# Kernel tuning notes

Measured on AMD Instinct MI355X. Metric: run time of the kernel, lower is better.

The kernel has to match this reference:

```python
import jax, jax.numpy as jnp
import numpy as np

# Constants from init_kwargs
NODE_BUDGET = 200.0
ALPHA = 0.5
COS_EPS = 1e-6

N, F = 200000, 256   # num_nodes, num_features
B = 1024             # batch_size (roots)
M = 500000           # candidate (u, batch) pairs this hop
E = 2000000          # frontier->candidate edges


def setup_inputs() -> dict:
    key = jax.random.key(0)
    ks = jax.random.split(key, 12)
    bound = 1.0 / np.sqrt(F)
    return {
        "x": jax.random.normal(ks[0], (N, F), dtype=jnp.float32),
        "w_ego_root": jax.random.uniform(ks[1], (F,), minval=-bound, maxval=bound, dtype=jnp.float32),
        "w_ego_u": jax.random.uniform(ks[2], (F,), minval=-bound, maxval=bound, dtype=jnp.float32),
        "w_layer_v": jax.random.uniform(ks[3], (F,), minval=-bound, maxval=bound, dtype=jnp.float32),
        "w_layer_u": jax.random.uniform(ks[4], (F,), minval=-bound, maxval=bound, dtype=jnp.float32),
        "n_imp": jax.random.uniform(ks[5], (N,), dtype=jnp.float32),
        "budgets": jnp.ones((B,), dtype=jnp.float32) * NODE_BUDGET,
        "batch_nodes": jax.random.randint(ks[6], (B,), 0, N, dtype=jnp.int32),
        "u_ids": jax.random.randint(ks[7], (M,), 0, N, dtype=jnp.int32),
        "batch_ptr": jnp.sort(jax.random.randint(ks[8], (M,), 0, B, dtype=jnp.int32)),
        "edge_src": jax.random.randint(ks[9], (E,), 0, B, dtype=jnp.int32),
        "edge_dst": jax.random.randint(ks[10], (E,), 0, M, dtype=jnp.int32),
    }


def reference(x, w_ego_root, w_ego_u, w_layer_v, w_layer_u, n_imp, budgets,
              batch_nodes, u_ids, batch_ptr, edge_src, edge_dst):
    # One hop of AdaptiveSampler.batch_wise_sampling score computation.
    # h_roots = x[batch_nodes] * w_ego_root  -> [B, F]
    x_roots = x[batch_nodes]                       # [B, F] gather
    h_roots = x_roots * w_ego_root                 # [B, F]
    xu = x[u_ids]                                  # [M, F] gather (dominant traffic)
    hu = xu * w_ego_u                              # [M, F]
    hr = h_roots[batch_ptr]                        # [M, F] gather

    # ego_score = cosine(h_roots[batch_ptr], x[u] * w_ego_u)
    dot = jnp.sum(hr * hu, axis=-1)                # [M]
    nr = jnp.linalg.norm(hr, axis=-1)
    nu = jnp.linalg.norm(hu, axis=-1)
    ego_score = dot / (jnp.maximum(nr, COS_EPS) * jnp.maximum(nu, COS_EPS))

    # layer_kernel: frontier projection scattered onto candidates via adjacency,
    # combined with the candidate projection (assumed tanh combine; see notes).
    sv = x_roots @ w_layer_v                       # [B]
    agg = jax.ops.segment_sum(sv[edge_src], edge_dst, num_segments=M)  # [M]
    su = xu @ w_layer_u                            # [M]
    layer_score = jnp.tanh(agg + su)               # [M]

    # p_u = (a*ego + (1-a)*layer) * n_imp[u] * (budget/node_budget)
    p_u = (ALPHA * ego_score + (1.0 - ALPHA) * layer_score) \
          * n_imp[u_ids] * (budgets[batch_ptr] / NODE_BUDGET)

    # per-batch normalizer (detached in original: .clone().detach())
    p_norm = jax.lax.stop_gradient(
        jax.ops.segment_max(p_u, batch_ptr, num_segments=B))  # [B]
    p_u = p_u / p_norm[batch_ptr] + 1.0
    # replace_nan(p_u, nan_to=0.0, inf_to=1.0)
    p_u = jnp.where(jnp.isnan(p_u), 0.0, jnp.where(jnp.isinf(p_u), 1.0, p_u))
    # p_clip = clamp(p_u, 1e-5, 1)
    p_clip = jnp.clip(p_u, 1e-5, 1.0)
    return p_clip
```

## Files before the change

kernel.cpp:

```cpp
#include <hip/hip_runtime.h>

#define F 256
#define NODE_BUDGET 200.0f
#define COS_EPS 1e-6f

__global__ __launch_bounds__(256) void root_kernel(
    const float* __restrict__ x,
    const float* __restrict__ w_ego_root,
    const float* __restrict__ w_ego_u,
    const float* __restrict__ w_layer_v,
    const float* __restrict__ budgets,
    const int* __restrict__ batch_nodes,
    float* __restrict__ g, float* __restrict__ nr,
    float* __restrict__ sv, float* __restrict__ bscale)
{
    __shared__ float red[2][4];
    int b = blockIdx.x;
    int f = threadIdx.x;
    int root = batch_nodes[b];
    float xf = x[(size_t)root * F + f];
    float hr = xf * w_ego_root[f];
    g[(size_t)b * F + f] = hr * w_ego_u[f];
    float a = hr * hr;
    float c = xf * w_layer_v[f];
    #pragma unroll
    for (int off = 32; off; off >>= 1) {
        a += __shfl_xor(a, off);
        c += __shfl_xor(c, off);
    }
    int lane = f & 63, wv = f >> 6;
    if (lane == 0) { red[0][wv] = a; red[1][wv] = c; }
    __syncthreads();
    if (f == 0) {
        float as = red[0][0] + red[0][1] + red[0][2] + red[0][3];
        float cs = red[1][0] + red[1][1] + red[1][2] + red[1][3];
        nr[b] = sqrtf(as);
        sv[b] = cs;
        bscale[b] = budgets[b] * (1.0f / NODE_BUDGET);
    }
}

__global__ __launch_bounds__(256) void edge_kernel(
    const int* __restrict__ edge_src, const int* __restrict__ edge_dst,
    const float* __restrict__ sv, float* __restrict__ agg, int E)
{
    int i = blockIdx.x * 256 + threadIdx.x;
    int stride = gridDim.x * 256;
    for (; i < E; i += stride)
        atomicAdd(&agg[edge_dst[i]], sv[edge_src[i]]);
}

__global__ __launch_bounds__(256) void cand_kernel(
    const float* __restrict__ x,
    const int* __restrict__ u_ids, const int* __restrict__ batch_ptr,
    const float* __restrict__ g, const float* __restrict__ nr,
    const float* __restrict__ bscale, const float* __restrict__ agg,
    const float* __restrict__ w_ego_u, const float* __restrict__ w_layer_u,
    const float* __restrict__ n_imp,
    float* __restrict__ p_out, int M)
{
    int tid = threadIdx.x;
    int lane = tid & 63;
    int sub = lane >> 4;
    int sl = lane & 15;
    int m = blockIdx.x * 16 + (tid >> 6) * 4 + sub;
    if (m >= M) return;
    int u = u_ids[m];
    int b = batch_ptr[m];
    const float4* xr = (const float4*)(x + (size_t)u * F);
    const float4* gr = (const float4*)(g + (size_t)b * F);
    const float4* weu = (const float4*)w_ego_u;
    const float4* wlu = (const float4*)w_layer_u;
    float acc = 0.0f;
    float a2  = 0.0f;
    float su  = 0.0f;
    #pragma unroll
    for (int p = 0; p < 4; ++p) {
        float4 xv = xr[p * 16 + sl];
        float4 gv = gr[p * 16 + sl];
        float4 wu = weu[p * 16 + sl];
        float4 wl = wlu[p * 16 + sl];
        acc += xv.x * gv.x + xv.y * gv.y + xv.z * gv.z + xv.w * gv.w;
        float h0 = xv.x * wu.x, h1 = xv.y * wu.y, h2 = xv.z * wu.z, h3 = xv.w * wu.w;
        a2  += h0 * h0 + h1 * h1 + h2 * h2 + h3 * h3;
        su  += xv.x * wl.x + xv.y * wl.y + xv.z * wl.z + xv.w * wl.w;
    }
    #pragma unroll
    for (int off = 8; off; off >>= 1) {
        acc += __shfl_xor(acc, off);
        a2  += __shfl_xor(a2, off);
        su  += __shfl_xor(su, off);
    }
    if (sl == 0) {
        float nu = sqrtf(a2);
        float ego = acc / (fmaxf(nr[b], COS_EPS) * fmaxf(nu, COS_EPS));
        float layer = tanhf(agg[m] + su);
        float p = (0.5f * ego + 0.5f * layer) * n_imp[u] * bscale[b];
        p_out[m] = p;
    }
}

__global__ __launch_bounds__(256) void seg_norm_kernel(
    const int* __restrict__ batch_ptr, float* __restrict__ out, int M)
{
    int b = blockIdx.x;
    int lo = 0, hi = M;
    while (lo < hi) { int mid = (lo + hi) >> 1; if (batch_ptr[mid] < b) lo = mid + 1; else hi = mid; }
    int start = lo;
    hi = M;
    while (lo < hi) { int mid = (lo + hi) >> 1; if (batch_ptr[mid] <= b) lo = mid + 1; else hi = mid; }
    int end = lo;
    float mx = -INFINITY;
    for (int i = start + threadIdx.x; i < end; i += 256)
        mx = fmaxf(mx, out[i]);
    #pragma unroll
    for (int off = 32; off; off >>= 1)
        mx = fmaxf(mx, __shfl_xor(mx, off));
    __shared__ float red[4];
    __shared__ float s_pn;
    int lane = threadIdx.x & 63, wv = threadIdx.x >> 6;
    if (lane == 0) red[wv] = mx;
    __syncthreads();
    if (threadIdx.x == 0)
        s_pn = fmaxf(fmaxf(red[0], red[1]), fmaxf(red[2], red[3]));
    __syncthreads();
    float pn = s_pn;
    for (int i = start + threadIdx.x; i < end; i += 256) {
        float v = out[i] / pn + 1.0f;
        if (isnan(v)) v = 0.0f;
        else if (isinf(v)) v = 1.0f;
        out[i] = fminf(fmaxf(v, 1e-5f), 1.0f);
    }
}

extern "C" void kernel_launch(void* const* d_in, const int* in_sizes, int n_in,
                              void* d_out, int out_size, void* d_ws, size_t ws_size,
                              hipStream_t stream) {
    const float* x          = (const float*)d_in[0];
    const float* w_ego_root = (const float*)d_in[1];
    const float* w_ego_u    = (const float*)d_in[2];
    const float* w_layer_v  = (const float*)d_in[3];
    const float* w_layer_u  = (const float*)d_in[4];
    const float* n_imp      = (const float*)d_in[5];
    const float* budgets    = (const float*)d_in[6];
    const int* batch_nodes = (const int*)d_in[7];
    const int* u_ids       = (const int*)d_in[8];
    const int* batch_ptr   = (const int*)d_in[9];
    const int* edge_src    = (const int*)d_in[10];
    const int* edge_dst    = (const int*)d_in[11];
    float* out = (float*)d_out;

    int B = in_sizes[7];
    int M = in_sizes[8];
    int E = in_sizes[10];

    float* ws = (float*)d_ws;
    size_t off = 0;
    float* agg = ws + off;                          off += (size_t)((M + 3) & ~3);
    size_t zero_bytes = off * sizeof(float);
    float* g       = ws + off;                      off += (size_t)B * F;
    float* nr      = ws + off;                      off += (size_t)((B + 3) & ~3);
    float* sv      = ws + off;                      off += (size_t)((B + 3) & ~3);
    float* bscale  = ws + off;                      off += (size_t)((B + 3) & ~3);

    hipMemsetAsync(d_ws, 0, zero_bytes, stream);

    root_kernel<<<B, 256, 0, stream>>>(x, w_ego_root, w_ego_u, w_layer_v,
                                       budgets, batch_nodes, g, nr, sv, bscale);
    edge_kernel<<<2048, 256, 0, stream>>>(edge_src, edge_dst, sv, agg, E);
    cand_kernel<<<(M + 15) / 16, 256, 0, stream>>>(x, u_ids, batch_ptr, g, nr,
                                                   bscale, agg, w_ego_u, w_layer_u,
                                                   n_imp, out, M);
    seg_norm_kernel<<<B, 256, 0, stream>>>(batch_ptr, out, M);
}
```

Measured before the change: 465.4 us.

## Group candidates by node via linked lists to reuse each x row

Builds per-node linked lists of candidate indices with atomicExch, then runs one 16-lane group per node. Each group loads the node's feature row once, computes its norm and layer projection once, and walks the list to compute the cosine against each root row. This cuts repeated gathers of x rows: with M=500k draws over N=200k nodes, many rows are duplicated, and the old path re-read x once per candidate. In exchange it adds a list-building pass, an extra memset, and serial pointer-chasing with uneven per-node work. Precomputing the inverse root norm is a small extra change.

```diff
diff --git a/kernel.cpp b/kernel.cpp
--- a/kernel.cpp
+++ b/kernel.cpp
@@ -11,7 +11,7 @@
     const float* __restrict__ w_layer_v,
     const float* __restrict__ budgets,
     const int* __restrict__ batch_nodes,
-    float* __restrict__ g, float* __restrict__ nr,
+    float* __restrict__ g, float* __restrict__ nrinv,
     float* __restrict__ sv, float* __restrict__ bscale)
 {
     __shared__ float red[2][4];
@@ -34,10 +34,20 @@
     if (f == 0) {
         float as = red[0][0] + red[0][1] + red[0][2] + red[0][3];
         float cs = red[1][0] + red[1][1] + red[1][2] + red[1][3];
-        nr[b] = sqrtf(as);
+        nrinv[b] = 1.0f / fmaxf(sqrtf(as), COS_EPS);
         sv[b] = cs;
         bscale[b] = budgets[b] * (1.0f / NODE_BUDGET);
     }
+}
+
+__global__ __launch_bounds__(256) void build_lists_kernel(
+    const int* __restrict__ u_ids, int* __restrict__ head,
+    int* __restrict__ next, int M)
+{
+    int i = blockIdx.x * 256 + threadIdx.x;
+    if (i >= M) return;
+    int u = u_ids[i];
+    next[i] = atomicExch(&head[u], i);
 }
 
 __global__ __launch_bounds__(256) void edge_kernel(
@@ -50,53 +60,68 @@
         atomicAdd(&agg[edge_dst[i]], sv[edge_src[i]]);
 }
 
-__global__ __launch_bounds__(256) void cand_kernel(
+__global__ __launch_bounds__(256) void cand_list_kernel(
     const float* __restrict__ x,
-    const int* __restrict__ u_ids, const int* __restrict__ batch_ptr,
-    const float* __restrict__ g, const float* __restrict__ nr,
+    const int* __restrict__ head, const int* __restrict__ next,
+    const int* __restrict__ batch_ptr,
+    const float* __restrict__ g, const float* __restrict__ nrinv,
     const float* __restrict__ bscale, const float* __restrict__ agg,
     const float* __restrict__ w_ego_u, const float* __restrict__ w_layer_u,
     const float* __restrict__ n_imp,
-    float* __restrict__ p_out, int M)
+    float* __restrict__ p_out, int N)
 {
     int tid = threadIdx.x;
     int lane = tid & 63;
     int sub = lane >> 4;
     int sl = lane & 15;
-    int m = blockIdx.x * 16 + (tid >> 6) * 4 + sub;
-    if (m >= M) return;
-    int u = u_ids[m];
-    int b = batch_ptr[m];
-    const float4* xr = (const float4*)(x + (size_t)u * F);
-    const float4* gr = (const float4*)(g + (size_t)b * F);
+    int n = blockIdx.x * 16 + (tid >> 6) * 4 + sub;
+    if (n >= N) return;
+    int m = head[n];
+    if (m < 0) return;
+
+    const float4* xr  = (const float4*)(x + (size_t)n * F);
     const float4* weu = (const float4*)w_ego_u;
     const float4* wlu = (const float4*)w_layer_u;
-    float acc = 0.0f;
-    float a2  = 0.0f;
-    float su  = 0.0f;
-    #pragma unroll
-    for (int p = 0; p < 4; ++p) {
-        float4 xv = xr[p * 16 + sl];
-        float4 gv = gr[p * 16 + sl];
-        float4 wu = weu[p * 16 + sl];
-        float4 wl = wlu[p * 16 + sl];
-        acc += xv.x * gv.x + xv.y * gv.y + xv.z * gv.z + xv.w * gv.w;
-        float h0 = xv.x * wu.x, h1 = xv.y * wu.y, h2 = xv.z * wu.z, h3 = xv.w * wu.w;
-        a2  += h0 * h0 + h1 * h1 + h2 * h2 + h3 * h3;
-        su  += xv.x * wl.x + xv.y * wl.y + xv.z * wl.z + xv.w * wl.w;
+
+    float4 xv0 = xr[sl], xv1 = xr[16 + sl], xv2 = xr[32 + sl], xv3 = xr[48 + sl];
+    float a2 = 0.0f, su = 0.0f;
+    {
+        float4 wu, wl, xv;
+        #define ACCUM(XV, P) \
+            xv = XV; wu = weu[(P)*16 + sl]; wl = wlu[(P)*16 + sl]; \
+            { float h0 = xv.x*wu.x, h1 = xv.y*wu.y, h2 = xv.z*wu.z, h3 = xv.w*wu.w; \
+              a2 += h0*h0 + h1*h1 + h2*h2 + h3*h3; \
+              su += xv.x*wl.x + xv.y*wl.y + xv.z*wl.z + xv.w*wl.w; }
+        ACCUM(xv0, 0) ACCUM(xv1, 1) ACCUM(xv2, 2) ACCUM(xv3, 3)
+        #undef ACCUM
     }
     #pragma unroll
     for (int off = 8; off; off >>= 1) {
-        acc += __shfl_xor(acc, off);
-        a2  += __shfl_xor(a2, off);
-        su  += __shfl_xor(su, off);
-    }
-    if (sl == 0) {
-        float nu = sqrtf(a2);
-        float ego = acc / (fmaxf(nr[b], COS_EPS) * fmaxf(nu, COS_EPS));
-        float layer = tanhf(agg[m] + su);
-        float p = (0.5f * ego + 0.5f * layer) * n_imp[u] * bscale[b];
-        p_out[m] = p;
+        a2 += __shfl_xor(a2, off);
+        su += __shfl_xor(su, off);
+    }
+    float inv_nu = 1.0f / fmaxf(sqrtf(a2), COS_EPS);
+    float imp = n_imp[n];
+
+    while (m >= 0) {
+        int mn = next[m];
+        int b = batch_ptr[m];
+        float ag = agg[m];
+        const float4* gr = (const float4*)(g + (size_t)b * F);
+        float4 g0 = gr[sl], g1 = gr[16 + sl], g2 = gr[32 + sl], g3 = gr[48 + sl];
+        float acc = xv0.x*g0.x + xv0.y*g0.y + xv0.z*g0.z + xv0.w*g0.w
+                  + xv1.x*g1.x + xv1.y*g1.y + xv1.z*g1.z + xv1.w*g1.w
+                  + xv2.x*g2.x + xv2.y*g2.y + xv2.z*g2.z + xv2.w*g2.w
+                  + xv3.x*g3.x + xv3.y*g3.y + xv3.z*g3.z + xv3.w*g3.w;
+        #pragma unroll
+        for (int off = 8; off; off >>= 1)
+            acc += __shfl_xor(acc, off);
+        if (sl == 0) {
+            float ego = acc * inv_nu * nrinv[b];
+            float layer = tanhf(ag + su);
+            p_out[m] = (0.5f * ego + 0.5f * layer) * imp * bscale[b];
+        }
+        m = mn;
     }
 }
 
@@ -150,6 +175,7 @@
     const int* edge_dst    = (const int*)d_in[11];
     float* out = (float*)d_out;
 
+    int N = in_sizes[5];
     int B = in_sizes[7];
     int M = in_sizes[8];
     int E = in_sizes[10];
@@ -159,17 +185,22 @@
     float* agg = ws + off;                          off += (size_t)((M + 3) & ~3);
     size_t zero_bytes = off * sizeof(float);
     float* g       = ws + off;                      off += (size_t)B * F;
-    float* nr      = ws + off;                      off += (size_t)((B + 3) & ~3);
+    float* nrinv   = ws + off;                      off += (size_t)((B + 3) & ~3);
     float* sv      = ws + off;                      off += (size_t)((B + 3) & ~3);
     float* bscale  = ws + off;                      off += (size_t)((B + 3) & ~3);
+    int* head      = (int*)(ws + off);              off += (size_t)((N + 3) & ~3);
+    int* next      = (int*)(ws + off);              off += (size_t)((M + 3) & ~3);
 
     hipMemsetAsync(d_ws, 0, zero_bytes, stream);
+    hipMemsetAsync(head, 0xFF, (size_t)N * sizeof(int), stream);
 
     root_kernel<<<B, 256, 0, stream>>>(x, w_ego_root, w_ego_u, w_layer_v,
-                                       budgets, batch_nodes, g, nr, sv, bscale);
+                                       budgets, batch_nodes, g, nrinv, sv, bscale);
+    build_lists_kernel<<<(M + 255) / 256, 256, 0, stream>>>(u_ids, head, next, M);
     edge_kernel<<<2048, 256, 0, stream>>>(edge_src, edge_dst, sv, agg, E);
-    cand_kernel<<<(M + 15) / 16, 256, 0, stream>>>(x, u_ids, batch_ptr, g, nr,
-                                                   bscale, agg, w_ego_u, w_layer_u,
-                                                   n_imp, out, M);
+    cand_list_kernel<<<(N + 15) / 16, 256, 0, stream>>>(x, head, next, batch_ptr,
+                                                        g, nrinv, bscale, agg,
+                                                        w_ego_u, w_layer_u, n_imp,
+                                                        out, N);
     seg_norm_kernel<<<B, 256, 0, stream>>>(batch_ptr, out, M);
 }
```

New measurement: 487.6 us. 4.8% more time.

## Bucket candidates by node id to improve cache locality of x row gathers

Applied to the files above, without the earlier changes.

Adds a scatter pass that buckets candidate indices into 32-node groups, using fixed-capacity slots plus an overflow list. The candidate kernel then walks this permutation, so rows of x for nearby node ids are read close together in time and can hit in L2/MALL instead of costing random HBM traffic. It also precomputes the reciprocal root norm. The price is an extra atomic scatter kernel, a memset of the perm buffer, many idle lanes from empty slots (S = 6250*128 = 800k slots for 500k items), and scattered writes to p_out.

```diff
diff --git a/kernel.cpp b/kernel.cpp
--- a/kernel.cpp
+++ b/kernel.cpp
@@ -3,6 +3,10 @@
 #define F 256
 #define NODE_BUDGET 200.0f
 #define COS_EPS 1e-6f
+
+#define BSHIFT 5
+#define PERM_CAP 128
+#define OVF_BLOCKS 64
 
 __global__ __launch_bounds__(256) void root_kernel(
     const float* __restrict__ x,
@@ -11,7 +15,7 @@
     const float* __restrict__ w_layer_v,
     const float* __restrict__ budgets,
     const int* __restrict__ batch_nodes,
-    float* __restrict__ g, float* __restrict__ nr,
+    float* __restrict__ g, float* __restrict__ nrinv,
     float* __restrict__ sv, float* __restrict__ bscale)
 {
     __shared__ float red[2][4];
@@ -34,10 +38,25 @@
     if (f == 0) {
         float as = red[0][0] + red[0][1] + red[0][2] + red[0][3];
         float cs = red[1][0] + red[1][1] + red[1][2] + red[1][3];
-        nr[b] = sqrtf(as);
+        nrinv[b] = 1.0f / fmaxf(sqrtf(as), COS_EPS);
         sv[b] = cs;
         bscale[b] = budgets[b] * (1.0f / NODE_BUDGET);
     }
+}
+
+__global__ __launch_bounds__(256) void scatter_kernel(
+    const int* __restrict__ u_ids, int* __restrict__ bcnt,
+    int* __restrict__ perm, int* __restrict__ ovf, int* __restrict__ ovf_cnt,
+    int M)
+{
+    int m = blockIdx.x * 256 + threadIdx.x;
+    if (m >= M) return;
+    int bk = u_ids[m] >> BSHIFT;
+    int t = atomicAdd(&bcnt[bk], 1);
+    if (t < PERM_CAP)
+        perm[(bk << 7) + t] = m;
+    else
+        ovf[atomicAdd(ovf_cnt, 1)] = m;
 }
 
 __global__ __launch_bounds__(256) void edge_kernel(
@@ -50,30 +69,22 @@
         atomicAdd(&agg[edge_dst[i]], sv[edge_src[i]]);
 }
 
-__global__ __launch_bounds__(256) void cand_kernel(
+__device__ __forceinline__ void process_cand(
+    int m, int sl,
     const float* __restrict__ x,
     const int* __restrict__ u_ids, const int* __restrict__ batch_ptr,
-    const float* __restrict__ g, const float* __restrict__ nr,
+    const float* __restrict__ g, const float* __restrict__ nrinv,
     const float* __restrict__ bscale, const float* __restrict__ agg,
     const float* __restrict__ w_ego_u, const float* __restrict__ w_layer_u,
-    const float* __restrict__ n_imp,
-    float* __restrict__ p_out, int M)
-{
-    int tid = threadIdx.x;
-    int lane = tid & 63;
-    int sub = lane >> 4;
-    int sl = lane & 15;
-    int m = blockIdx.x * 16 + (tid >> 6) * 4 + sub;
-    if (m >= M) return;
+    const float* __restrict__ n_imp, float* __restrict__ p_out)
+{
     int u = u_ids[m];
     int b = batch_ptr[m];
-    const float4* xr = (const float4*)(x + (size_t)u * F);
-    const float4* gr = (const float4*)(g + (size_t)b * F);
+    const float4* xr  = (const float4*)(x + (size_t)u * F);
+    const float4* gr  = (const float4*)(g + (size_t)b * F);
     const float4* weu = (const float4*)w_ego_u;
     const float4* wlu = (const float4*)w_layer_u;
-    float acc = 0.0f;
-    float a2  = 0.0f;
-    float su  = 0.0f;
+    float acc = 0.0f, a2 = 0.0f, su = 0.0f;
     #pragma unroll
     for (int p = 0; p < 4; ++p) {
         float4 xv = xr[p * 16 + sl];
@@ -93,10 +104,41 @@
     }
     if (sl == 0) {
         float nu = sqrtf(a2);
-        float ego = acc / (fmaxf(nr[b], COS_EPS) * fmaxf(nu, COS_EPS));
+        float ego = acc * nrinv[b] / fmaxf(nu, COS_EPS);
         float layer = tanhf(agg[m] + su);
-        float p = (0.5f * ego + 0.5f * layer) * n_imp[u] * bscale[b];
-        p_out[m] = p;
+        p_out[m] = (0.5f * ego + 0.5f * layer) * n_imp[u] * bscale[b];
+    }
+}
+
+__global__ __launch_bounds__(256) void cand_perm_kernel(
+    const float* __restrict__ x,
+    const int* __restrict__ perm,
+    const int* __restrict__ u_ids, const int* __restrict__ batch_ptr,
+    const float* __restrict__ g, const float* __restrict__ nrinv,
+    const float* __restrict__ bscale, const float* __restrict__ agg,
+    const float* __restrict__ w_ego_u, const float* __restrict__ w_layer_u,
+    const float* __restrict__ n_imp,
+    const int* __restrict__ ovf, const int* __restrict__ ovf_cnt,
+    float* __restrict__ p_out, int S, int mainBlocks)
+{
+    int tid = threadIdx.x;
+    int lane = tid & 63;
+    int sub = lane >> 4;
+    int sl = lane & 15;
+    if (blockIdx.x < (unsigned)mainBlocks) {
+        int i = blockIdx.x * 16 + (tid >> 6) * 4 + sub;
+        if (i >= S) return;
+        int m = perm[i];
+        if (m < 0) return;
+        process_cand(m, sl, x, u_ids, batch_ptr, g, nrinv, bscale, agg,
+                     w_ego_u, w_layer_u, n_imp, p_out);
+    } else {
+        int cnt = *ovf_cnt;
+        int i = (blockIdx.x - mainBlocks) * 16 + (tid >> 6) * 4 + sub;
+        int stride = OVF_BLOCKS * 16;
+        for (; i < cnt; i += stride)
+            process_cand(ovf[i], sl, x, u_ids, batch_ptr, g, nrinv, bscale, agg,
+                         w_ego_u, w_layer_u, n_imp, p_out);
     }
 }
 
@@ -150,26 +192,38 @@
     const int* edge_dst    = (const int*)d_in[11];
     float* out = (float*)d_out;
 
+    int N = in_sizes[5];
     int B = in_sizes[7];
     int M = in_sizes[8];
     int E = in_sizes[10];
 
+    int NB = (N + (1 << BSHIFT) - 1) >> BSHIFT;
+    int S = NB * PERM_CAP;
+
     float* ws = (float*)d_ws;
     size_t off = 0;
-    float* agg = ws + off;                          off += (size_t)((M + 3) & ~3);
+    float* agg   = ws + off;                off += (size_t)((M + 3) & ~3);
+    int* bcnt    = (int*)(ws + off);        off += (size_t)((NB + 3) & ~3);
+    int* ovf_cnt = (int*)(ws + off);        off += 4;
     size_t zero_bytes = off * sizeof(float);
-    float* g       = ws + off;                      off += (size_t)B * F;
-    float* nr      = ws + off;                      off += (size_t)((B + 3) & ~3);
-    float* sv      = ws + off;                      off += (size_t)((B + 3) & ~3);
-    float* bscale  = ws + off;                      off += (size_t)((B + 3) & ~3);
+    float* g      = ws + off;               off += (size_t)B * F;
+    float* nrinv  = ws + off;               off += (size_t)((B + 3) & ~3);
+    float* sv     = ws + off;               off += (size_t)((B + 3) & ~3);
+    float* bscale = ws + off;               off += (size_t)((B + 3) & ~3);
+    int* perm     = (int*)(ws + off);       off += (size_t)S;
+    int* ovf      = (int*)(ws + off);       off += (size_t)((M + 3) & ~3);
 
     hipMemsetAsync(d_ws, 0, zero_bytes, stream);
-
+    hipMemsetAsync(perm, 0xFF, (size_t)S * sizeof(int), stream);
+
+    scatter_kernel<<<(M + 255) / 256, 256, 0, stream>>>(u_ids, bcnt, perm, ovf,
+                                                        ovf_cnt, M);
     root_kernel<<<B, 256, 0, stream>>>(x, w_ego_root, w_ego_u, w_layer_v,
-                                       budgets, batch_nodes, g, nr, sv, bscale);
+                                       budgets, batch_nodes, g, nrinv, sv, bscale);
     edge_kernel<<<2048, 256, 0, stream>>>(edge_src, edge_dst, sv, agg, E);
-    cand_kernel<<<(M + 15) / 16, 256, 0, stream>>>(x, u_ids, batch_ptr, g, nr,
-                                                   bscale, agg, w_ego_u, w_layer_u,
-                                                   n_imp, out, M);
+    int mainBlocks = (S + 15) / 16;
+    cand_perm_kernel<<<mainBlocks + OVF_BLOCKS, 256, 0, stream>>>(
+        x, perm, u_ids, batch_ptr, g, nrinv, bscale, agg,
+        w_ego_u, w_layer_u, n_imp, ovf, ovf_cnt, out, S, mainBlocks);
     seg_norm_kernel<<<B, 256, 0, stream>>>(batch_ptr, out, M);
 }
```

Result: slower. 594.0 us (+27.6%).

## Sort candidates by node id to reuse gathered feature rows

Applied to the files above, without the earlier changes.

Builds a counting sort of candidate indices by u_ids (histogram, tiled scan, atomic scatter) and processes candidates in sorted order so duplicate x rows are read back-to-back and hit cache. Block IDs are remapped into contiguous chunks per group of 8 to keep neighbouring work on the same cache domain. Also precomputes the inverse root norm. This adds several small kernels and scattered per-candidate metadata reads and output writes in exchange for less HBM traffic on the dominant gather.

```diff
diff --git a/kernel.cpp b/kernel.cpp
--- a/kernel.cpp
+++ b/kernel.cpp
@@ -3,6 +3,7 @@
 #define F 256
 #define NODE_BUDGET 200.0f
 #define COS_EPS 1e-6f
+#define TILE 2048
 
 __global__ __launch_bounds__(256) void root_kernel(
     const float* __restrict__ x,
@@ -11,7 +12,7 @@
     const float* __restrict__ w_layer_v,
     const float* __restrict__ budgets,
     const int* __restrict__ batch_nodes,
-    float* __restrict__ g, float* __restrict__ nr,
+    float* __restrict__ g, float* __restrict__ nrinv,
     float* __restrict__ sv, float* __restrict__ bscale)
 {
     __shared__ float red[2][4];
@@ -34,10 +35,75 @@
     if (f == 0) {
         float as = red[0][0] + red[0][1] + red[0][2] + red[0][3];
         float cs = red[1][0] + red[1][1] + red[1][2] + red[1][3];
-        nr[b] = sqrtf(as);
+        nrinv[b] = 1.0f / fmaxf(sqrtf(as), COS_EPS);
         sv[b] = cs;
         bscale[b] = budgets[b] * (1.0f / NODE_BUDGET);
     }
+}
+
+__global__ __launch_bounds__(256) void hist_kernel(
+    const int* __restrict__ u_ids, int* __restrict__ cnt, int M)
+{
+    int m = blockIdx.x * 256 + threadIdx.x;
+    if (m < M) atomicAdd(&cnt[u_ids[m]], 1);
+}
+
+__global__ __launch_bounds__(256) void scan_tiles_kernel(
+    const int* __restrict__ cnt, int* __restrict__ exc,
+    int* __restrict__ tsum, int N)
+{
+    __shared__ int sh[256];
+    int t = threadIdx.x;
+    int base = blockIdx.x * TILE + t * 8;
+    int v[8];
+    int run = 0;
+    #pragma unroll
+    for (int k = 0; k < 8; ++k) {
+        int c = (base + k < N) ? cnt[base + k] : 0;
+        v[k] = run; run += c;
+    }
+    sh[t] = run;
+    __syncthreads();
+    for (int off = 1; off < 256; off <<= 1) {
+        int val = (t >= off) ? sh[t - off] : 0;
+        __syncthreads();
+        sh[t] += val;
+        __syncthreads();
+    }
+    int texc = sh[t] - run;
+    #pragma unroll
+    for (int k = 0; k < 8; ++k)
+        if (base + k < N) exc[base + k] = v[k] + texc;
+    if (t == 255) tsum[blockIdx.x] = sh[255];
+}
+
+__global__ void scan_sums_kernel(int* __restrict__ tsum, int NT)
+{
+    if (blockIdx.x == 0 && threadIdx.x == 0) {
+        int run = 0;
+        for (int i = 0; i < NT; ++i) { int c = tsum[i]; tsum[i] = run; run += c; }
+    }
+}
+
+__global__ __launch_bounds__(256) void add_offsets_kernel(
+    const int* __restrict__ exc, const int* __restrict__ tsum,
+    int* __restrict__ cursor, int N)
+{
+    int base = blockIdx.x * TILE + threadIdx.x * 8;
+    int add = tsum[blockIdx.x];
+    #pragma unroll
+    for (int k = 0; k < 8; ++k)
+        if (base + k < N) cursor[base + k] = exc[base + k] + add;
+}
+
+__global__ __launch_bounds__(256) void scatter_sorted_kernel(
+    const int* __restrict__ u_ids, int* __restrict__ cursor,
+    int* __restrict__ sorted_m, int M)
+{
+    int m = blockIdx.x * 256 + threadIdx.x;
+    if (m >= M) return;
+    int pos = atomicAdd(&cursor[u_ids[m]], 1);
+    sorted_m[pos] = m;
 }
 
 __global__ __launch_bounds__(256) void edge_kernel(
@@ -50,30 +116,35 @@
         atomicAdd(&agg[edge_dst[i]], sv[edge_src[i]]);
 }
 
-__global__ __launch_bounds__(256) void cand_kernel(
+__global__ __launch_bounds__(256) void cand_sorted_kernel(
     const float* __restrict__ x,
+    const int* __restrict__ sorted_m,
     const int* __restrict__ u_ids, const int* __restrict__ batch_ptr,
-    const float* __restrict__ g, const float* __restrict__ nr,
+    const float* __restrict__ g, const float* __restrict__ nrinv,
     const float* __restrict__ bscale, const float* __restrict__ agg,
     const float* __restrict__ w_ego_u, const float* __restrict__ w_layer_u,
     const float* __restrict__ n_imp,
     float* __restrict__ p_out, int M)
 {
+    int G = gridDim.x;
+    int bid = blockIdx.x;
+    int q = G >> 3, r = G & 7, xc = bid & 7, j = bid >> 3;
+    int wg = (xc < r ? xc * (q + 1) : r * (q + 1) + (xc - r) * q) + j;
+
     int tid = threadIdx.x;
     int lane = tid & 63;
     int sub = lane >> 4;
     int sl = lane & 15;
-    int m = blockIdx.x * 16 + (tid >> 6) * 4 + sub;
-    if (m >= M) return;
+    int i = wg * 16 + (tid >> 6) * 4 + sub;
+    if (i >= M) return;
+    int m = sorted_m[i];
     int u = u_ids[m];
     int b = batch_ptr[m];
-    const float4* xr = (const float4*)(x + (size_t)u * F);
-    const float4* gr = (const float4*)(g + (size_t)b * F);
+    const float4* xr  = (const float4*)(x + (size_t)u * F);
+    const float4* gr  = (const float4*)(g + (size_t)b * F);
     const float4* weu = (const float4*)w_ego_u;
     const float4* wlu = (const float4*)w_layer_u;
-    float acc = 0.0f;
-    float a2  = 0.0f;
-    float su  = 0.0f;
+    float acc = 0.0f, a2 = 0.0f, su = 0.0f;
     #pragma unroll
     for (int p = 0; p < 4; ++p) {
         float4 xv = xr[p * 16 + sl];
@@ -93,10 +164,9 @@
     }
     if (sl == 0) {
         float nu = sqrtf(a2);
-        float ego = acc / (fmaxf(nr[b], COS_EPS) * fmaxf(nu, COS_EPS));
+        float ego = acc * nrinv[b] / fmaxf(nu, COS_EPS);
         float layer = tanhf(agg[m] + su);
-        float p = (0.5f * ego + 0.5f * layer) * n_imp[u] * bscale[b];
-        p_out[m] = p;
+        p_out[m] = (0.5f * ego + 0.5f * layer) * n_imp[u] * bscale[b];
     }
 }
 
@@ -150,26 +220,40 @@
     const int* edge_dst    = (const int*)d_in[11];
     float* out = (float*)d_out;
 
+    int N = in_sizes[5];
     int B = in_sizes[7];
     int M = in_sizes[8];
     int E = in_sizes[10];
 
+    int NT = (N + TILE - 1) / TILE;
+
     float* ws = (float*)d_ws;
     size_t off = 0;
-    float* agg = ws + off;                          off += (size_t)((M + 3) & ~3);
+    float* agg  = ws + off;                 off += (size_t)((M + 3) & ~3);
+    int* cnt    = (int*)(ws + off);         off += (size_t)((N + 3) & ~3);
     size_t zero_bytes = off * sizeof(float);
-    float* g       = ws + off;                      off += (size_t)B * F;
-    float* nr      = ws + off;                      off += (size_t)((B + 3) & ~3);
-    float* sv      = ws + off;                      off += (size_t)((B + 3) & ~3);
-    float* bscale  = ws + off;                      off += (size_t)((B + 3) & ~3);
+    float* g      = ws + off;               off += (size_t)B * F;
+    float* nrinv  = ws + off;               off += (size_t)((B + 3) & ~3);
+    float* sv     = ws + off;               off += (size_t)((B + 3) & ~3);
+    float* bscale = ws + off;               off += (size_t)((B + 3) & ~3);
+    int* exc      = (int*)(ws + off);       off += (size_t)((N + 3) & ~3);
+    int* tsum     = (int*)(ws + off);       off += (size_t)((NT + 3) & ~3);
+    int* cursor   = (int*)(ws + off);       off += (size_t)((N + 3) & ~3);
+    int* sorted_m = (int*)(ws + off);       off += (size_t)((M + 3) & ~3);
 
     hipMemsetAsync(d_ws, 0, zero_bytes, stream);
 
+    hist_kernel<<<(M + 255) / 256, 256, 0, stream>>>(u_ids, cnt, M);
+    scan_tiles_kernel<<<NT, 256, 0, stream>>>(cnt, exc, tsum, N);
+    scan_sums_kernel<<<1, 64, 0, stream>>>(tsum, NT);
+    add_offsets_kernel<<<NT, 256, 0, stream>>>(exc, tsum, cursor, N);
+    scatter_sorted_kernel<<<(M + 255) / 256, 256, 0, stream>>>(u_ids, cursor,
+                                                               sorted_m, M);
     root_kernel<<<B, 256, 0, stream>>>(x, w_ego_root, w_ego_u, w_layer_v,
-                                       budgets, batch_nodes, g, nr, sv, bscale);
+                                       budgets, batch_nodes, g, nrinv, sv, bscale);
     edge_kernel<<<2048, 256, 0, stream>>>(edge_src, edge_dst, sv, agg, E);
-    cand_kernel<<<(M + 15) / 16, 256, 0, stream>>>(x, u_ids, batch_ptr, g, nr,
-                                                   bscale, agg, w_ego_u, w_layer_u,
-                                                   n_imp, out, M);
+    cand_sorted_kernel<<<(M + 15) / 16, 256, 0, stream>>>(
+        x, sorted_m, u_ids, batch_ptr, g, nrinv, bscale, agg,
+        w_ego_u, w_layer_u, n_imp, out, M);
     seg_norm_kernel<<<B, 256, 0, stream>>>(batch_ptr, out, M);
 }
```

Measured after the change: 544.2 us. 1.17x slower.
